# Performance work log

Hardware: AMD Instinct MI355X
Metric: run time of the kernel (lower is better)

Reference implementation:

```python
import jax, jax.numpy as jnp
import numpy as np

ALPHA = 0.2  # LeakyReLU negative slope
NEG_INF = -9e15


def _xavier(key, shape, gain=1.414):
    fan_in, fan_out = shape[-2], shape[-1]
    lim = gain * np.sqrt(6.0 / (fan_in + fan_out))
    return jax.random.uniform(key, shape, jnp.float32, -lim, lim)


def setup_inputs() -> dict:
    key = jax.random.key(0)
    ks = jax.random.split(key, 8)
    B, N, Din, H, Dh, Do = 8, 1024, 256, 4, 128, 64
    x = jax.random.normal(ks[0], (B, N, Din), jnp.float32)
    adj = jax.random.randint(ks[1], (B, N, N), 0, 2).astype(jnp.int32)
    W_heads = _xavier(ks[2], (H, Din, Dh))                 # per-head W
    a_heads = _xavier(ks[3], (H, 2 * Dh, 1))[..., 0]       # per-head a, [H, 2*Dh]
    W_out = _xavier(ks[4], (H * Dh, Do))                   # out_att W
    a_out = _xavier(ks[5], (2 * Do, 1))[..., 0]            # out_att a, [2*Do]
    Wf = _xavier(ks[6], (Do, Do), gain=1.0)                # fc_out linear
    bf = jnp.zeros((Do,), jnp.float32)
    return {"x": x, "adj": adj, "W_heads": W_heads, "a_heads": a_heads,
            "W_out": W_out, "a_out": a_out, "Wf": Wf, "bf": bf}


def _leaky_relu(v):
    return jnp.where(v >= 0, v, ALPHA * v)


def _gat(h, adj, W, a):
    # h: [B,N,Fin], adj: [B,N,N], W: [Fin,Fout], a: [2*Fout]
    Wh = h @ W                                   # [B,N,F]
    F = W.shape[-1]
    # additive attention: e_ij = leakyrelu(a_src.Wh_i + a_dst.Wh_j)
    src = Wh @ a[:F]                             # [B,N]
    dst = Wh @ a[F:]                             # [B,N]
    e = _leaky_relu(src[:, :, None] + dst[:, None, :])   # [B,N,N]
    scores = jnp.where(adj > 0, e, NEG_INF)
    attn = jax.nn.softmax(scores, axis=-1)       # dropout is a no-op in eval
    return attn @ Wh                             # [B,N,F]


def reference(x, adj, W_heads, a_heads, W_out, a_out, Wf, bf):
    B, N, _ = x.shape
    H, _, Dh = W_heads.shape
    # multi-head GAT, heads vmapped over leading axis of W_heads / a_heads
    heads = jax.vmap(_gat, in_axes=(None, None, 0, 0))(x, adj, W_heads, a_heads)  # [H,B,N,Dh]
    xcat = jnp.moveaxis(heads, 0, 2).reshape(B, N, H * Dh)   # concat heads, dim=2
    out = jax.nn.elu(_gat(xcat, adj, W_out, a_out))           # [B,N,Do]
    out = jax.nn.relu(out @ Wf + bf)                          # fc_out (dropout no-op)
    return out
```

## Files before the change

kernel.cpp:

```cpp
#include <hip/hip_runtime.h>
#include <hip/hip_bf16.h>

#define BSZ 8
#define NN 1024
#define DIN 256
#define NH 4
#define DH 128
#define DOUT 64
#define RTOT (BSZ*NN)
#define FCAT (NH*DH)
#define ALPHA 0.2f

typedef unsigned short ushortT;
typedef __attribute__((ext_vector_type(8))) short bf16x8;
typedef __attribute__((ext_vector_type(4))) float f32x4;

static __device__ __forceinline__ ushortT f2bf(float f) {
    __hip_bfloat16 h = __float2bfloat16(f);
    return *reinterpret_cast<ushortT*>(&h);
}
static __device__ __forceinline__ float bfu2f(ushortT u) {
    return __uint_as_float(((unsigned)u) << 16);
}
static __device__ __forceinline__ void split2(float v, ushortT& hi, ushortT& lo) {
    hi = f2bf(v);
    lo = f2bf(v - bfu2f(hi));
}
static __device__ __forceinline__ void gload16(const ushortT* g, ushortT* l) {
    __builtin_amdgcn_global_load_lds(
        (const __attribute__((address_space(1))) unsigned int*)(const void*)g,
        (__attribute__((address_space(3))) unsigned int*)(void*)l, 16, 0, 0);
}

__global__ __launch_bounds__(256) void k_prepw(const float* __restrict__ W,
                                               const float* __restrict__ Wout,
                                               ushortT* __restrict__ WbTh, ushortT* __restrict__ WbTl,
                                               ushortT* __restrict__ WoTh, ushortT* __restrict__ WoTl) {
    const int g2 = blockIdx.x * 256 + threadIdx.x;
    if (g2 < NH * DH * DIN) {
        const int h = g2 >> 15, f = (g2 >> 8) & 127, k = g2 & 255;
        const int kt = k >> 6, k64 = k & 63;
        const float v = W[(size_t)h * DIN * DH + (size_t)k * DH + f];
        ushortT hi, lo; split2(v, hi, lo);
        const int idx = ((h * 4 + kt) * 128 + f) * 64 + k64;
        WbTh[idx] = hi; WbTl[idx] = lo;
    } else {
        const int g3 = g2 - NH * DH * DIN;
        const int f = g3 >> 9, k = g3 & 511;
        const float v = Wout[(size_t)k * DOUT + f];
        ushortT hi, lo; split2(v, hi, lo);
        WoTh[g3] = hi; WoTl[g3] = lo;
    }
}

__global__ __launch_bounds__(512) void k_main(const float* __restrict__ x,
                                              const float* __restrict__ ah_,
                                              const ushortT* __restrict__ WbTh,
                                              const ushortT* __restrict__ WbTl,
                                              const int* __restrict__ adj,
                                              unsigned* __restrict__ adjbit,
                                              ushortT* __restrict__ WhT,
                                              float* __restrict__ src1,
                                              float* __restrict__ dst1) {
    __shared__ ushortT Ah[128 * 64], Al[128 * 64];
    __shared__ ushortT Bh[128 * 64], Bl[128 * 64];
    __shared__ float sred[8][32], dred[8][32];
    const int tid = threadIdx.x;
    if (blockIdx.x >= 256) {
        const int g = (blockIdx.x - 256) * 512 + tid;
        const int row = g >> 5, w = g & 31;
        const int4* p = (const int4*)(adj + (size_t)row * NN + w * 32);
        unsigned m = 0;
#pragma unroll
        for (int q = 0; q < 8; ++q) {
            const int4 v = p[q];
            m |= (v.x > 0 ? 1u : 0u) << (q * 4 + 0);
            m |= (v.y > 0 ? 1u : 0u) << (q * 4 + 1);
            m |= (v.z > 0 ? 1u : 0u) << (q * 4 + 2);
            m |= (v.w > 0 ? 1u : 0u) << (q * 4 + 3);
        }
        adjbit[g] = m;
        return;
    }
    const int lane = tid & 63, wave = tid >> 6;
    const int h = blockIdx.x >> 6, mt = blockIdx.x & 63;
    const int r0 = mt * 128, b = r0 >> 10, jr = r0 & 1023;
    const int m16 = lane & 15, quad = lane >> 4;
    const int mg = wave >> 1, fg = wave & 1;
    const int arow = tid >> 2, apart = tid & 3;
    f32x4 acc[2][4];
#pragma unroll
    for (int a = 0; a < 2; ++a)
#pragma unroll
        for (int c = 0; c < 4; ++c) acc[a][c] = (f32x4){0.f, 0.f, 0.f, 0.f};

    for (int kt = 0; kt < 4; ++kt) {
        __syncthreads();
        const ushortT* planeH = WbTh + (size_t)((h * 4 + kt) * 128) * 64;
        const ushortT* planeL = WbTl + (size_t)((h * 4 + kt) * 128) * 64;
#pragma unroll
        for (int half = 0; half < 2; ++half) {
            const int f = wave * 16 + half * 8 + (lane >> 3);
            const int sc = (lane & 7) ^ (f & 7);
            gload16(planeH + (size_t)f * 64 + sc * 8, Bh + (wave * 16 + half * 8) * 64);
            gload16(planeL + (size_t)f * 64 + sc * 8, Bl + (wave * 16 + half * 8) * 64);
        }
        {
            const float4* xs = (const float4*)(x + (size_t)(r0 + arow) * DIN + kt * 64 + apart * 16);
            union { ushortT u[16]; uint4 q[2]; } th, tl;
#pragma unroll
            for (int e = 0; e < 4; ++e) {
                const float4 v = xs[e];
                split2(v.x, th.u[e * 4 + 0], tl.u[e * 4 + 0]);
                split2(v.y, th.u[e * 4 + 1], tl.u[e * 4 + 1]);
                split2(v.z, th.u[e * 4 + 2], tl.u[e * 4 + 2]);
                split2(v.w, th.u[e * 4 + 3], tl.u[e * 4 + 3]);
            }
            const int s0 = (2 * apart) ^ (arow & 7), s1 = (2 * apart + 1) ^ (arow & 7);
            *(uint4*)&Ah[arow * 64 + s0 * 8] = th.q[0];
            *(uint4*)&Ah[arow * 64 + s1 * 8] = th.q[1];
            *(uint4*)&Al[arow * 64 + s0 * 8] = tl.q[0];
            *(uint4*)&Al[arow * 64 + s1 * 8] = tl.q[1];
        }
        __syncthreads();
#pragma unroll
        for (int ks = 0; ks < 2; ++ks) {
            bf16x8 a_h[2], a_l[2], b_h[4], b_l[4];
#pragma unroll
            for (int ms = 0; ms < 2; ++ms) {
                const int row = (mg * 2 + ms) * 16 + m16;
                const int cl = (ks * 4 + quad) ^ (row & 7);
                a_h[ms] = *(const bf16x8*)&Ah[row * 64 + cl * 8];
                a_l[ms] = *(const bf16x8*)&Al[row * 64 + cl * 8];
            }
#pragma unroll
            for (int fs = 0; fs < 4; ++fs) {
                const int row = (fg * 4 + fs) * 16 + m16;
                const int cl = (ks * 4 + quad) ^ (row & 7);
                b_h[fs] = *(const bf16x8*)&Bh[row * 64 + cl * 8];
                b_l[fs] = *(const bf16x8*)&Bl[row * 64 + cl * 8];
            }
#pragma unroll
            for (int ms = 0; ms < 2; ++ms)
#pragma unroll
                for (int fs = 0; fs < 4; ++fs) {
                    acc[ms][fs] = __builtin_amdgcn_mfma_f32_16x16x32_bf16(a_h[ms], b_h[fs], acc[ms][fs], 0, 0, 0);
                    acc[ms][fs] = __builtin_amdgcn_mfma_f32_16x16x32_bf16(a_h[ms], b_l[fs], acc[ms][fs], 0, 0, 0);
                    acc[ms][fs] = __builtin_amdgcn_mfma_f32_16x16x32_bf16(a_l[ms], b_h[fs], acc[ms][fs], 0, 0, 0);
                }
        }
    }
    float sacc[2][4] = {{0,0,0,0},{0,0,0,0}}, dacc[2][4] = {{0,0,0,0},{0,0,0,0}};
#pragma unroll
    for (int ms = 0; ms < 2; ++ms)
#pragma unroll
        for (int fs = 0; fs < 4; ++fs) {
            const int fl = (fg * 4 + fs) * 16 + m16;
            const float a_s = ah_[h * 2 * DH + fl];
            const float a_d = ah_[h * 2 * DH + DH + fl];
            union { ushortT u[4]; uint2 q; } tw;
#pragma unroll
            for (int reg = 0; reg < 4; ++reg) {
                const float v = acc[ms][fs][reg];
                sacc[ms][reg] += v * a_s;
                dacc[ms][reg] += v * a_d;
                tw.u[reg] = f2bf(v);
            }
            *(uint2*)(WhT + ((size_t)((b * NH + h) * DH + fl)) * NN + jr + (mg * 2 + ms) * 16 + quad * 4) = tw.q;
        }
#pragma unroll
    for (int ms = 0; ms < 2; ++ms) {
#pragma unroll
        for (int reg = 0; reg < 4; ++reg) {
            float s = sacc[ms][reg], d = dacc[ms][reg];
#pragma unroll
            for (int o = 8; o > 0; o >>= 1) {
                s += __shfl_xor(s, o, 64);
                d += __shfl_xor(d, o, 64);
            }
            if (m16 == 0) {
                sred[wave][ms * 16 + quad * 4 + reg] = s;
                dred[wave][ms * 16 + quad * 4 + reg] = d;
            }
        }
    }
    __syncthreads();
    if (tid < 128) {
        const int mgr = tid >> 5, idx = tid & 31;
        src1[h * RTOT + r0 + tid] = sred[mgr * 2][idx] + sred[mgr * 2 + 1][idx];
        dst1[h * RTOT + r0 + tid] = dred[mgr * 2][idx] + dred[mgr * 2 + 1][idx];
    }
}

__global__ __launch_bounds__(512) void k_attn1(const unsigned* __restrict__ adjbit,
                                               const ushortT* __restrict__ WhT,
                                               const float* __restrict__ src1,
                                               const float* __restrict__ dst1,
                                               ushortT* __restrict__ xcatH,
                                               ushortT* __restrict__ xcatL) {
    __shared__ ushortT As[64 * 64];
    __shared__ ushortT Bs[128 * 64];
    __shared__ unsigned maskS[64 * 32];
    __shared__ float dstv[NN];
    __shared__ float srcv[64], rowinv[64], red8[8];
    const int tid = threadIdx.x, lane = tid & 63, wave = tid >> 6;
    const int bh = blockIdx.x & 31, it = blockIdx.x >> 5;
    const int b = bh >> 2, h = bh & 3;
    const int i0 = it * 64;
    const int m16 = lane & 15, quad = lane >> 4;
    const int mg = wave >> 1, fg = wave & 1;

    const unsigned* mbase = adjbit + (size_t)(b * NN + i0) * 32;
#pragma unroll
    for (int k2 = 0; k2 < 4; ++k2) maskS[tid + 512 * k2] = mbase[tid + 512 * k2];
    const float d0 = dst1[h * RTOT + b * NN + tid];
    const float d1 = dst1[h * RTOT + b * NN + tid + 512];
    dstv[tid] = d0; dstv[tid + 512] = d1;
    if (tid < 64) srcv[tid] = src1[h * RTOT + b * NN + i0 + tid];
    float lm = fmaxf(d0, d1);
#pragma unroll
    for (int o = 32; o > 0; o >>= 1) lm = fmaxf(lm, __shfl_xor(lm, o, 64));
    if (lane == 0) red8[wave] = lm;
    __syncthreads();
    const float dmax = fmaxf(fmaxf(fmaxf(red8[0], red8[1]), fmaxf(red8[2], red8[3])),
                             fmaxf(fmaxf(red8[4], red8[5]), fmaxf(red8[6], red8[7])));

    const int arow = tid >> 3, apart = tid & 7;
    const float si = srcv[arow];
    float mrow = si + dmax;
    mrow = mrow >= 0.f ? mrow : ALPHA * mrow;
    float fsum = 0.f;

    const ushortT* Bbase = WhT + (size_t)(bh * DH) * NN;
    f32x4 acc[4];
#pragma unroll
    for (int c = 0; c < 4; ++c) acc[c] = (f32x4){0.f, 0.f, 0.f, 0.f};

    for (int kt = 0; kt < 16; ++kt) {
        __syncthreads();
#pragma unroll
        for (int half = 0; half < 2; ++half) {
            const int f = wave * 16 + half * 8 + (lane >> 3);
            gload16(Bbase + (size_t)f * NN + kt * 64 + (((lane & 7) ^ (f & 7)) * 8),
                    Bs + (wave * 16 + half * 8) * 64);
        }
        {
            const unsigned w0 = maskS[arow * 32 + kt * 2 + (apart >> 2)];
            const int bb = (apart & 3) * 8;
            union { ushortT u[8]; uint4 q; } tw;
#pragma unroll
            for (int e4 = 0; e4 < 2; ++e4) {
                const float4 dv = *(const float4*)&dstv[kt * 64 + apart * 8 + e4 * 4];
                const float vv[4] = {dv.x, dv.y, dv.z, dv.w};
#pragma unroll
                for (int e = 0; e < 4; ++e) {
                    float v = si + vv[e];
                    v = v >= 0.f ? v : ALPHA * v;
                    const unsigned bit = (w0 >> (bb + e4 * 4 + e)) & 1u;
                    const float p = bit ? __expf(v - mrow) : 0.f;
                    fsum += p;
                    tw.u[e4 * 4 + e] = f2bf(p);
                }
            }
            *(uint4*)&As[arow * 64 + (apart ^ (arow & 7)) * 8] = tw.q;
        }
        __syncthreads();
#pragma unroll
        for (int ks = 0; ks < 2; ++ks) {
            const int rowa = mg * 16 + m16;
            const int cla = (ks * 4 + quad) ^ (rowa & 7);
            const bf16x8 afr = *(const bf16x8*)&As[rowa * 64 + cla * 8];
#pragma unroll
            for (int fs = 0; fs < 4; ++fs) {
                const int rowb = fg * 64 + fs * 16 + m16;
                const int clb = (ks * 4 + quad) ^ (rowb & 7);
                const bf16x8 bfr = *(const bf16x8*)&Bs[rowb * 64 + clb * 8];
                acc[fs] = __builtin_amdgcn_mfma_f32_16x16x32_bf16(afr, bfr, acc[fs], 0, 0, 0);
            }
        }
    }
#pragma unroll
    for (int o = 1; o < 8; o <<= 1) fsum += __shfl_xor(fsum, o, 64);
    if ((lane & 7) == 0) rowinv[arow] = 1.f / fsum;
    __syncthreads();
    float rv[4];
#pragma unroll
    for (int reg = 0; reg < 4; ++reg) rv[reg] = rowinv[mg * 16 + quad * 4 + reg];
#pragma unroll
    for (int fs = 0; fs < 4; ++fs) {
        const int f = h * DH + fg * 64 + fs * 16 + m16;
#pragma unroll
        for (int reg = 0; reg < 4; ++reg) {
            const int i = i0 + mg * 16 + quad * 4 + reg;
            const float v = acc[fs][reg] * rv[reg];
            const size_t idx = (size_t)(b * NN + i) * FCAT + f;
            ushortT hi, lo; split2(v, hi, lo);
            xcatH[idx] = hi;
            xcatL[idx] = lo;
        }
    }
}

__global__ __launch_bounds__(256) void k_wh2(const ushortT* __restrict__ xcatH,
                                             const ushortT* __restrict__ xcatL,
                                             const ushortT* __restrict__ WoTh,
                                             const ushortT* __restrict__ WoTl,
                                             const float* __restrict__ aout,
                                             ushortT* __restrict__ Wh2T,
                                             float* __restrict__ src2,
                                             float* __restrict__ dst2) {
    __shared__ float sred[4][16], dred[4][16];
    const int tid = threadIdx.x;
    const int r0  = blockIdx.x * 16;
    const int b   = r0 >> 10, jr = r0 & 1023;
    const int lane = tid & 63, wave = tid >> 6;
    const int quad = lane >> 4, n = lane & 15;
    const int f0 = wave * 16;
    const ushortT* ahp = xcatH + (size_t)(r0 + n) * FCAT + quad * 8;
    const ushortT* alp = xcatL + (size_t)(r0 + n) * FCAT + quad * 8;
    const ushortT* bhp = WoTh + (size_t)(f0 + n) * FCAT + quad * 8;
    const ushortT* blp = WoTl + (size_t)(f0 + n) * FCAT + quad * 8;
    f32x4 acc = {0.f, 0.f, 0.f, 0.f};
#pragma unroll
    for (int s = 0; s < 16; ++s) {
        const int off = 32 * s;
        const bf16x8 ah = *(const bf16x8*)(ahp + off);
        const bf16x8 al = *(const bf16x8*)(alp + off);
        const bf16x8 bh = *(const bf16x8*)(bhp + off);
        const bf16x8 bl = *(const bf16x8*)(blp + off);
        acc = __builtin_amdgcn_mfma_f32_16x16x32_bf16(ah, bh, acc, 0, 0, 0);
        acc = __builtin_amdgcn_mfma_f32_16x16x32_bf16(ah, bl, acc, 0, 0, 0);
        acc = __builtin_amdgcn_mfma_f32_16x16x32_bf16(al, bh, acc, 0, 0, 0);
    }
    const int f = f0 + n;
    const float a_s = aout[f], a_d = aout[DOUT + f];
    float sv[4], dv[4];
    union { ushortT u[4]; uint2 q; } tw;
#pragma unroll
    for (int reg = 0; reg < 4; ++reg) {
        const float v = acc[reg];
        sv[reg] = v * a_s; dv[reg] = v * a_d;
        tw.u[reg] = f2bf(v);
    }
    *(uint2*)(Wh2T + ((size_t)(b * DOUT + f)) * NN + jr + quad * 4) = tw.q;
#pragma unroll
    for (int reg = 0; reg < 4; ++reg) {
#pragma unroll
        for (int o = 8; o > 0; o >>= 1) {
            sv[reg] += __shfl_xor(sv[reg], o, 64);
            dv[reg] += __shfl_xor(dv[reg], o, 64);
        }
        if (n == 0) { sred[wave][quad * 4 + reg] = sv[reg]; dred[wave][quad * 4 + reg] = dv[reg]; }
    }
    __syncthreads();
    if (tid < 16) {
        src2[r0 + tid] = sred[0][tid] + sred[1][tid] + sred[2][tid] + sred[3][tid];
        dst2[r0 + tid] = dred[0][tid] + dred[1][tid] + dred[2][tid] + dred[3][tid];
    }
}

__global__ __launch_bounds__(256) void k_attn2(const unsigned* __restrict__ adjbit,
                                               const ushortT* __restrict__ Wh2T,
                                               const float* __restrict__ src2,
                                               const float* __restrict__ dst2,
                                               const float* __restrict__ Wf,
                                               const float* __restrict__ bfv,
                                               float* __restrict__ out) {
    __shared__ ushortT As[32 * 64];
    __shared__ ushortT Bs[64 * 64];
    __shared__ unsigned maskS[32 * 32];
    __shared__ float dstv[NN];
    __shared__ ushortT Wfh[64 * 64], Wfl[64 * 64];
    __shared__ float t2s[32 * 68];
    __shared__ float srcv[32], rowinv[32], red4[4];
    const int tid = threadIdx.x, lane = tid & 63, wave = tid >> 6;
    const int b = blockIdx.x & 7, it = blockIdx.x >> 3;
    const int i0 = it * 32;
    const int m16 = lane & 15, quad = lane >> 4;

    const unsigned* mbase = adjbit + (size_t)(b * NN + i0) * 32;
#pragma unroll
    for (int k2 = 0; k2 < 4; ++k2) maskS[tid + 256 * k2] = mbase[tid + 256 * k2];
    float lm = -INFINITY;
#pragma unroll
    for (int k2 = 0; k2 < 4; ++k2) {
        const float d = dst2[b * NN + tid + 256 * k2];
        dstv[tid + 256 * k2] = d;
        lm = fmaxf(lm, d);
    }
    if (tid < 32) srcv[tid] = src2[b * NN + i0 + tid];
    {
        const int c = tid & 63, kc = (tid >> 6) * 16;
        union { ushortT u[16]; uint4 q[2]; } th, tl;
#pragma unroll
        for (int e = 0; e < 16; ++e)
            split2(Wf[(size_t)(kc + e) * DOUT + c], th.u[e], tl.u[e]);
        const int s0 = ((tid >> 6) * 2) ^ (c & 7), s1 = ((tid >> 6) * 2 + 1) ^ (c & 7);
        *(uint4*)&Wfh[c * 64 + s0 * 8] = th.q[0];
        *(uint4*)&Wfh[c * 64 + s1 * 8] = th.q[1];
        *(uint4*)&Wfl[c * 64 + s0 * 8] = tl.q[0];
        *(uint4*)&Wfl[c * 64 + s1 * 8] = tl.q[1];
    }
#pragma unroll
    for (int o = 32; o > 0; o >>= 1) lm = fmaxf(lm, __shfl_xor(lm, o, 64));
    if (lane == 0) red4[wave] = lm;
    __syncthreads();
    const float dmax = fmaxf(fmaxf(red4[0], red4[1]), fmaxf(red4[2], red4[3]));

    const int arow = tid >> 3, apart = tid & 7;
    const float si = srcv[arow];
    float mrow = si + dmax;
    mrow = mrow >= 0.f ? mrow : ALPHA * mrow;
    float fsum = 0.f;

    const int mfrag = wave >> 1, fh = wave & 1;
    const ushortT* Bbase = Wh2T + (size_t)(b * DOUT) * NN;
    f32x4 acc[2] = {(f32x4){0.f,0.f,0.f,0.f}, (f32x4){0.f,0.f,0.f,0.f}};

    for (int kt = 0; kt < 16; ++kt) {
        __syncthreads();
#pragma unroll
        for (int half = 0; half < 2; ++half) {
            const int f = wave * 16 + half * 8 + (lane >> 3);
            gload16(Bbase + (size_t)f * NN + kt * 64 + (((lane & 7) ^ (f & 7)) * 8),
                    Bs + (wave * 16 + half * 8) * 64);
        }
        {
            const unsigned w0 = maskS[arow * 32 + kt * 2 + (apart >> 2)];
            const int bb = (apart & 3) * 8;
            union { ushortT u[8]; uint4 q; } tw;
#pragma unroll
            for (int e4 = 0; e4 < 2; ++e4) {
                const float4 dv = *(const float4*)&dstv[kt * 64 + apart * 8 + e4 * 4];
                const float vv[4] = {dv.x, dv.y, dv.z, dv.w};
#pragma unroll
                for (int e = 0; e < 4; ++e) {
                    float v = si + vv[e];
                    v = v >= 0.f ? v : ALPHA * v;
                    const unsigned bit = (w0 >> (bb + e4 * 4 + e)) & 1u;
                    const float p = bit ? __expf(v - mrow) : 0.f;
                    fsum += p;
                    tw.u[e4 * 4 + e] = f2bf(p);
                }
            }
            *(uint4*)&As[arow * 64 + (apart ^ (arow & 7)) * 8] = tw.q;
        }
        __syncthreads();
#pragma unroll
        for (int ks = 0; ks < 2; ++ks) {
            const int rowa = mfrag * 16 + m16;
            const int cla = (ks * 4 + quad) ^ (rowa & 7);
            const bf16x8 afr = *(const bf16x8*)&As[rowa * 64 + cla * 8];
#pragma unroll
            for (int ff = 0; ff < 2; ++ff) {
                const int rowb = (fh * 2 + ff) * 16 + m16;
                const int clb = (ks * 4 + quad) ^ (rowb & 7);
                const bf16x8 bfr = *(const bf16x8*)&Bs[rowb * 64 + clb * 8];
                acc[ff] = __builtin_amdgcn_mfma_f32_16x16x32_bf16(afr, bfr, acc[ff], 0, 0, 0);
            }
        }
    }
#pragma unroll
    for (int o = 1; o < 8; o <<= 1) fsum += __shfl_xor(fsum, o, 64);
    if ((lane & 7) == 0) rowinv[arow] = 1.f / fsum;
    __syncthreads();
#pragma unroll
    for (int ff = 0; ff < 2; ++ff) {
#pragma unroll
        for (int reg = 0; reg < 4; ++reg) {
            const int row = mfrag * 16 + quad * 4 + reg;
            float v = acc[ff][reg] * rowinv[row];
            v = v > 0.f ? v : (__expf(v) - 1.f);
            t2s[row * 68 + (fh * 2 + ff) * 16 + m16] = v;
        }
    }
    __syncthreads();
    const int mf = wave >> 1, nh = wave & 1;
    f32x4 oacc[2];
#pragma unroll
    for (int g = 0; g < 2; ++g) {
        const float bias = bfv[(nh * 2 + g) * 16 + m16];
        oacc[g] = (f32x4){bias, bias, bias, bias};
    }
#pragma unroll
    for (int ks = 0; ks < 2; ++ks) {
        const int rowa = mf * 16 + m16;
        const float4 fA = *(const float4*)&t2s[rowa * 68 + ks * 32 + quad * 8];
        const float4 fB = *(const float4*)&t2s[rowa * 68 + ks * 32 + quad * 8 + 4];
        union { ushortT u[8]; bf16x8 v; } a_h, a_l;
        const float av[8] = {fA.x, fA.y, fA.z, fA.w, fB.x, fB.y, fB.z, fB.w};
#pragma unroll
        for (int e = 0; e < 8; ++e) split2(av[e], a_h.u[e], a_l.u[e]);
#pragma unroll
        for (int g = 0; g < 2; ++g) {
            const int rowc = (nh * 2 + g) * 16 + m16;
            const int cl = (ks * 4 + quad) ^ (rowc & 7);
            const bf16x8 b_h = *(const bf16x8*)&Wfh[rowc * 64 + cl * 8];
            const bf16x8 b_l = *(const bf16x8*)&Wfl[rowc * 64 + cl * 8];
            oacc[g] = __builtin_amdgcn_mfma_f32_16x16x32_bf16(a_h.v, b_h, oacc[g], 0, 0, 0);
            oacc[g] = __builtin_amdgcn_mfma_f32_16x16x32_bf16(a_h.v, b_l, oacc[g], 0, 0, 0);
            oacc[g] = __builtin_amdgcn_mfma_f32_16x16x32_bf16(a_l.v, b_h, oacc[g], 0, 0, 0);
        }
    }
#pragma unroll
    for (int g = 0; g < 2; ++g) {
        const int c = (nh * 2 + g) * 16 + m16;
#pragma unroll
        for (int reg = 0; reg < 4; ++reg) {
            const int i = i0 + mf * 16 + quad * 4 + reg;
            out[(size_t)(b * NN + i) * DOUT + c] = fmaxf(oacc[g][reg], 0.f);
        }
    }
}

extern "C" void kernel_launch(void* const* d_in, const int* in_sizes, int n_in,
                              void* d_out, int out_size, void* d_ws, size_t ws_size,
                              hipStream_t stream) {
    const float* x   = (const float*)d_in[0];
    const int*   adj = (const int*)d_in[1];
    const float* Wh  = (const float*)d_in[2];
    const float* ah  = (const float*)d_in[3];
    const float* Wo  = (const float*)d_in[4];
    const float* ao  = (const float*)d_in[5];
    const float* Wf  = (const float*)d_in[6];
    const float* bf  = (const float*)d_in[7];
    float* out = (float*)d_out;

    float* ws    = (float*)d_ws;
    float* src1  = ws;
    float* dst1  = src1 + NH * RTOT;
    float* src2  = dst1 + NH * RTOT;
    float* dst2  = src2 + RTOT;
    ushortT* WhT   = (ushortT*)(dst2 + RTOT);
    ushortT* Wh2T  = WhT + (size_t)RTOT * FCAT;
    ushortT* xcatH = Wh2T + (size_t)RTOT * DOUT;
    ushortT* xcatL = xcatH + (size_t)RTOT * FCAT;
    ushortT* WbTh  = xcatL + (size_t)RTOT * FCAT;
    ushortT* WbTl  = WbTh + NH * DH * DIN;
    ushortT* WoTh  = WbTl + NH * DH * DIN;
    ushortT* WoTl  = WoTh + DOUT * FCAT;
    unsigned* adjbit = (unsigned*)(WoTl + DOUT * FCAT);

    hipLaunchKernelGGL(k_prepw, dim3((NH * DH * DIN + DOUT * FCAT) / 256), dim3(256), 0, stream,
                       Wh, Wo, WbTh, WbTl, WoTh, WoTl);
    hipLaunchKernelGGL(k_main,  dim3(768), dim3(512), 0, stream,
                       x, ah, WbTh, WbTl, adj, adjbit, WhT, src1, dst1);
    hipLaunchKernelGGL(k_attn1, dim3(512), dim3(512), 0, stream,
                       adjbit, WhT, src1, dst1, xcatH, xcatL);
    hipLaunchKernelGGL(k_wh2,   dim3(RTOT / 16), dim3(256), 0, stream,
                       xcatH, xcatL, WoTh, WoTl, ao, Wh2T, src2, dst2);
    hipLaunchKernelGGL(k_attn2, dim3(256), dim3(256), 0, stream,
                       adjbit, Wh2T, src2, dst2, Wf, bf, out);
}
```

Before: 164.9 us.

## Store head concat as single bf16 and tile second projection through LDS

The head outputs from the first attention stage are now stored as a single bf16 array instead of a hi/lo split pair. This halves the xcat write and read traffic and drops one MFMA per k-step in the second projection. The second projection kernel is restructured to stage 32-row A tiles and 64-wide hi/lo W_out tiles in swizzled LDS, with 256 blocks instead of 512 direct-from-global blocks. The cost is lower precision in the concatenated activations, which can shift the output error.

```diff
diff --git a/kernel.cpp b/kernel.cpp
--- a/kernel.cpp
+++ b/kernel.cpp
@@ -196,8 +196,7 @@
                                                const ushortT* __restrict__ WhT,
                                                const float* __restrict__ src1,
                                                const float* __restrict__ dst1,
-                                               ushortT* __restrict__ xcatH,
-                                               ushortT* __restrict__ xcatL) {
+                                               ushortT* __restrict__ xcat) {
     __shared__ ushortT As[64 * 64];
     __shared__ ushortT Bs[128 * 64];
     __shared__ unsigned maskS[64 * 32];
@@ -292,57 +291,74 @@
 #pragma unroll
         for (int reg = 0; reg < 4; ++reg) {
             const int i = i0 + mg * 16 + quad * 4 + reg;
-            const float v = acc[fs][reg] * rv[reg];
-            const size_t idx = (size_t)(b * NN + i) * FCAT + f;
-            ushortT hi, lo; split2(v, hi, lo);
-            xcatH[idx] = hi;
-            xcatL[idx] = lo;
-        }
-    }
-}
-
-__global__ __launch_bounds__(256) void k_wh2(const ushortT* __restrict__ xcatH,
-                                             const ushortT* __restrict__ xcatL,
+            xcat[(size_t)(b * NN + i) * FCAT + f] = f2bf(acc[fs][reg] * rv[reg]);
+        }
+    }
+}
+
+__global__ __launch_bounds__(256) void k_wh2(const ushortT* __restrict__ xcat,
                                              const ushortT* __restrict__ WoTh,
                                              const ushortT* __restrict__ WoTl,
                                              const float* __restrict__ aout,
                                              ushortT* __restrict__ Wh2T,
                                              float* __restrict__ src2,
                                              float* __restrict__ dst2) {
+    __shared__ ushortT As[32 * 64];
+    __shared__ ushortT Bh[64 * 64], Bl[64 * 64];
     __shared__ float sred[4][16], dred[4][16];
-    const int tid = threadIdx.x;
-    const int r0  = blockIdx.x * 16;
-    const int b   = r0 >> 10, jr = r0 & 1023;
-    const int lane = tid & 63, wave = tid >> 6;
-    const int quad = lane >> 4, n = lane & 15;
-    const int f0 = wave * 16;
-    const ushortT* ahp = xcatH + (size_t)(r0 + n) * FCAT + quad * 8;
-    const ushortT* alp = xcatL + (size_t)(r0 + n) * FCAT + quad * 8;
-    const ushortT* bhp = WoTh + (size_t)(f0 + n) * FCAT + quad * 8;
-    const ushortT* blp = WoTl + (size_t)(f0 + n) * FCAT + quad * 8;
-    f32x4 acc = {0.f, 0.f, 0.f, 0.f};
-#pragma unroll
-    for (int s = 0; s < 16; ++s) {
-        const int off = 32 * s;
-        const bf16x8 ah = *(const bf16x8*)(ahp + off);
-        const bf16x8 al = *(const bf16x8*)(alp + off);
-        const bf16x8 bh = *(const bf16x8*)(bhp + off);
-        const bf16x8 bl = *(const bf16x8*)(blp + off);
-        acc = __builtin_amdgcn_mfma_f32_16x16x32_bf16(ah, bh, acc, 0, 0, 0);
-        acc = __builtin_amdgcn_mfma_f32_16x16x32_bf16(ah, bl, acc, 0, 0, 0);
-        acc = __builtin_amdgcn_mfma_f32_16x16x32_bf16(al, bh, acc, 0, 0, 0);
-    }
-    const int f = f0 + n;
-    const float a_s = aout[f], a_d = aout[DOUT + f];
-    float sv[4], dv[4];
-    union { ushortT u[4]; uint2 q; } tw;
-#pragma unroll
-    for (int reg = 0; reg < 4; ++reg) {
-        const float v = acc[reg];
-        sv[reg] = v * a_s; dv[reg] = v * a_d;
-        tw.u[reg] = f2bf(v);
-    }
-    *(uint2*)(Wh2T + ((size_t)(b * DOUT + f)) * NN + jr + quad * 4) = tw.q;
+    const int tid = threadIdx.x, lane = tid & 63, wave = tid >> 6;
+    const int r0 = blockIdx.x * 32;
+    const int b = r0 >> 10, jr = r0 & 1023;
+    const int m16 = lane & 15, quad = lane >> 4;
+    const int mg = wave >> 1, fg = wave & 1;
+    f32x4 acc[2] = {(f32x4){0.f,0.f,0.f,0.f}, (f32x4){0.f,0.f,0.f,0.f}};
+
+    for (int kt = 0; kt < 8; ++kt) {
+        __syncthreads();
+        {
+            const int row = wave * 8 + (lane >> 3);
+            const int sc = (lane & 7) ^ (row & 7);
+            gload16(xcat + (size_t)(r0 + row) * FCAT + kt * 64 + sc * 8, As + wave * 8 * 64);
+        }
+#pragma unroll
+        for (int half = 0; half < 2; ++half) {
+            const int f = wave * 16 + half * 8 + (lane >> 3);
+            const int sc = (lane & 7) ^ (f & 7);
+            gload16(WoTh + (size_t)f * FCAT + kt * 64 + sc * 8, Bh + (wave * 16 + half * 8) * 64);
+            gload16(WoTl + (size_t)f * FCAT + kt * 64 + sc * 8, Bl + (wave * 16 + half * 8) * 64);
+        }
+        __syncthreads();
+#pragma unroll
+        for (int ks = 0; ks < 2; ++ks) {
+            const int rowa = mg * 16 + m16;
+            const int cla = (ks * 4 + quad) ^ (rowa & 7);
+            const bf16x8 afr = *(const bf16x8*)&As[rowa * 64 + cla * 8];
+#pragma unroll
+            for (int ff = 0; ff < 2; ++ff) {
+                const int rowb = fg * 32 + ff * 16 + m16;
+                const int clb = (ks * 4 + quad) ^ (rowb & 7);
+                const bf16x8 b_h = *(const bf16x8*)&Bh[rowb * 64 + clb * 8];
+                const bf16x8 b_l = *(const bf16x8*)&Bl[rowb * 64 + clb * 8];
+                acc[ff] = __builtin_amdgcn_mfma_f32_16x16x32_bf16(afr, b_h, acc[ff], 0, 0, 0);
+                acc[ff] = __builtin_amdgcn_mfma_f32_16x16x32_bf16(afr, b_l, acc[ff], 0, 0, 0);
+            }
+        }
+    }
+    float sv[4] = {0, 0, 0, 0}, dv[4] = {0, 0, 0, 0};
+#pragma unroll
+    for (int ff = 0; ff < 2; ++ff) {
+        const int f = fg * 32 + ff * 16 + m16;
+        const float a_s = aout[f], a_d = aout[DOUT + f];
+        union { ushortT u[4]; uint2 q; } tw;
+#pragma unroll
+        for (int reg = 0; reg < 4; ++reg) {
+            const float v = acc[ff][reg];
+            sv[reg] += v * a_s;
+            dv[reg] += v * a_d;
+            tw.u[reg] = f2bf(v);
+        }
+        *(uint2*)(Wh2T + ((size_t)(b * DOUT + f)) * NN + jr + mg * 16 + quad * 4) = tw.q;
+    }
 #pragma unroll
     for (int reg = 0; reg < 4; ++reg) {
 #pragma unroll
@@ -350,12 +366,13 @@
             sv[reg] += __shfl_xor(sv[reg], o, 64);
             dv[reg] += __shfl_xor(dv[reg], o, 64);
         }
-        if (n == 0) { sred[wave][quad * 4 + reg] = sv[reg]; dred[wave][quad * 4 + reg] = dv[reg]; }
-    }
-    __syncthreads();
-    if (tid < 16) {
-        src2[r0 + tid] = sred[0][tid] + sred[1][tid] + sred[2][tid] + sred[3][tid];
-        dst2[r0 + tid] = dred[0][tid] + dred[1][tid] + dred[2][tid] + dred[3][tid];
+        if (m16 == 0) { sred[wave][quad * 4 + reg] = sv[reg]; dred[wave][quad * 4 + reg] = dv[reg]; }
+    }
+    __syncthreads();
+    if (tid < 32) {
+        const int mgr = tid >> 4, idx = tid & 15;
+        src2[r0 + tid] = sred[mgr * 2][idx] + sred[mgr * 2 + 1][idx];
+        dst2[r0 + tid] = dred[mgr * 2][idx] + dred[mgr * 2 + 1][idx];
     }
 }
 
@@ -533,9 +550,8 @@
     float* dst2  = src2 + RTOT;
     ushortT* WhT   = (ushortT*)(dst2 + RTOT);
     ushortT* Wh2T  = WhT + (size_t)RTOT * FCAT;
-    ushortT* xcatH = Wh2T + (size_t)RTOT * DOUT;
-    ushortT* xcatL = xcatH + (size_t)RTOT * FCAT;
-    ushortT* WbTh  = xcatL + (size_t)RTOT * FCAT;
+    ushortT* xcat  = Wh2T + (size_t)RTOT * DOUT;
+    ushortT* WbTh  = xcat + (size_t)RTOT * FCAT;
     ushortT* WbTl  = WbTh + NH * DH * DIN;
     ushortT* WoTh  = WbTl + NH * DH * DIN;
     ushortT* WoTl  = WoTh + DOUT * FCAT;
@@ -546,9 +562,9 @@
     hipLaunchKernelGGL(k_main,  dim3(768), dim3(512), 0, stream,
                        x, ah, WbTh, WbTl, adj, adjbit, WhT, src1, dst1);
     hipLaunchKernelGGL(k_attn1, dim3(512), dim3(512), 0, stream,
-                       adjbit, WhT, src1, dst1, xcatH, xcatL);
-    hipLaunchKernelGGL(k_wh2,   dim3(RTOT / 16), dim3(256), 0, stream,
-                       xcatH, xcatL, WoTh, WoTl, ao, Wh2T, src2, dst2);
+                       adjbit, WhT, src1, dst1, xcat);
+    hipLaunchKernelGGL(k_wh2,   dim3(256), dim3(256), 0, stream,
+                       xcat, WoTh, WoTl, ao, Wh2T, src2, dst2);
     hipLaunchKernelGGL(k_attn2, dim3(256), dim3(256), 0, stream,
                        adjbit, Wh2T, src2, dst2, Wf, bf, out);
 }
```

Result: faster. 157.4 us (-4.5%).
